# Kernel optimization log

Measured on AMD Instinct MI355X. Metric: run time of the kernel, lower is better.

The kernel has to match this reference:

```python
import jax, jax.numpy as jnp
import numpy as np

N_HEAD = 16

def setup_inputs() -> dict:
    key = jax.random.key(0)
    kx, kq, kk, kv, kp = jax.random.split(key, 5)
    B, T, C = 4, 2048, 1024
    scale = 1.0 / np.sqrt(C)
    x = jax.random.normal(kx, (B, T, C), dtype=jnp.float32)
    Wq = jax.random.normal(kq, (C, C), dtype=jnp.float32) * scale
    Wk = jax.random.normal(kk, (C, C), dtype=jnp.float32) * scale
    Wv = jax.random.normal(kv, (C, C), dtype=jnp.float32) * scale
    Wp = jax.random.normal(kp, (C, C), dtype=jnp.float32) * scale
    return {"x": x, "Wq": Wq, "Wk": Wk, "Wv": Wv, "Wp": Wp}

def reference(x, Wq, Wk, Wv, Wp):
    B, T, C = x.shape
    H = N_HEAD
    D = C // H
    # projections (nn.Linear, no bias): x @ W^T
    q = (x @ Wq.T).reshape(B, T, H, D).transpose(0, 2, 1, 3)  # [B,H,T,D]
    k = (x @ Wk.T).reshape(B, T, H, D).transpose(0, 2, 1, 3)
    v = (x @ Wv.T).reshape(B, T, H, D).transpose(0, 2, 1, 3)
    att = jnp.einsum('bhqd,bhkd->bhqk', q, k) / jnp.sqrt(jnp.float32(D))
    causal = jnp.tril(jnp.ones((T, T), dtype=bool))
    att = jnp.where(causal, att, -jnp.inf)
    att = jax.nn.softmax(att, axis=-1)
    # dropout p=0.0 -> identity
    y = jnp.einsum('bhqk,bhkd->bhqd', att, v)  # [B,H,T,D]
    y = y.transpose(0, 2, 1, 3).reshape(B, T, C)
    return y @ Wp.T
```

## Files before the change

kernel.cpp:

```cpp
#include <hip/hip_runtime.h>

typedef __bf16 bfrag __attribute__((ext_vector_type(8)));
typedef __bf16 bh4 __attribute__((ext_vector_type(4)));
typedef float f4 __attribute__((ext_vector_type(4)));

#define AS1C(p) (const __attribute__((address_space(1))) void*)(p)
#define AS3(p)  (__attribute__((address_space(3))) void*)(p)

#define QSCALE 0.18033688011112042f

__device__ __forceinline__ void g2l16(const __bf16* g, __bf16* l) {
  __builtin_amdgcn_global_load_lds(AS1C(g), AS3(l), 16, 0, 0);
}

__global__ __launch_bounds__(256) void cvt5(
    const float* __restrict__ s0, const float* __restrict__ s1,
    const float* __restrict__ s2, const float* __restrict__ s3,
    const float* __restrict__ s4,
    __bf16* __restrict__ d0, __bf16* __restrict__ d1, __bf16* __restrict__ d2,
    __bf16* __restrict__ d3, __bf16* __restrict__ d4, long n0, long n1) {
  const float* s; __bf16* d; long n;
  switch (blockIdx.y) {
    case 0: s = s0; d = d0; n = n0; break;
    case 1: s = s1; d = d1; n = n1; break;
    case 2: s = s2; d = d2; n = n1; break;
    case 3: s = s3; d = d3; n = n1; break;
    default: s = s4; d = d4; n = n1; break;
  }
  long i = ((long)blockIdx.x * 256 + threadIdx.x) * 8;
  if (i >= n) return;
  float4 a = *(const float4*)(s + i);
  float4 b = *(const float4*)(s + i + 4);
  bfrag o;
  o[0] = (__bf16)a.x; o[1] = (__bf16)a.y; o[2] = (__bf16)a.z; o[3] = (__bf16)a.w;
  o[4] = (__bf16)b.x; o[5] = (__bf16)b.y; o[6] = (__bf16)b.z; o[7] = (__bf16)b.w;
  *(bfrag*)(d + i) = o;
}

#define BARR __builtin_amdgcn_s_barrier()
#define WAIT_LGKM { asm volatile("s_waitcnt lgkmcnt(0)" ::: "memory"); \
                    __builtin_amdgcn_sched_barrier(0); }
#define WAIT_VM(N) asm volatile("s_waitcnt vmcnt(" #N ")" ::: "memory")

template <int MODE>
__global__ __launch_bounds__(512, 2) void gemm_dp(
    const __bf16* __restrict__ A, const __bf16* __restrict__ Bw,
    __bf16* __restrict__ qb, __bf16* __restrict__ kb,
    __bf16* __restrict__ vt, float* __restrict__ Cf, int K) {
  __shared__ __bf16 lds[73728];
  __bf16* ldsA = lds;
  __bf16* ldsB = lds + 24576;
  const int tid = threadIdx.x;
  const int wave = tid >> 6, lane = tid & 63;
  const int lm = lane & 15, quad = lane >> 4;
  const int wm = wave >> 2, wn = wave & 3;
  const int bm = blockIdx.x * 128, bn = blockIdx.y * 256;
  const int srow = lane >> 3;
  const int scol = ((lane & 7) ^ srow) * 8;
  const int rsw = lm & 7;

#define STG_A9(sl, kt) { \
    const __bf16* gp_ = A + (long)(bm + wave * 16 + srow) * K + (kt) * 64 + scol; \
    __bf16* lp_ = ldsA + (sl) * 8192 + wave * 1024 + lane * 8; \
    g2l16(gp_, lp_); g2l16(gp_ + 8 * K, lp_ + 512); }
#define STG_B9(sl, kt, h) { \
    const __bf16* gp_ = Bw + (long)(bn + (h) * 128 + wave * 16 + srow) * K + (kt) * 64 + scol; \
    __bf16* lp_ = ldsB + (sl) * 16384 + (h) * 8192 + wave * 1024 + lane * 8; \
    g2l16(gp_, lp_); g2l16(gp_ + 8 * K, lp_ + 512); }
#define STG_TILE(sl, kt) { STG_A9(sl, kt); STG_B9(sl, kt, 0); STG_B9(sl, kt, 1); }

#define COMPUTE_HALF(sl) { \
    const __bf16* Ab_ = ldsA + (sl) * 8192 + (wm * 64 + lm) * 64; \
    const __bf16* Bb_ = ldsB + (sl) * 16384 + (wn * 64 + lm) * 64; \
    bfrag af_[4][2], bg_[2][2]; \
    _Pragma("unroll") for (int j_ = 0; j_ < 4; ++j_) \
      _Pragma("unroll") for (int kk_ = 0; kk_ < 2; ++kk_) \
        af_[j_][kk_] = *(const bfrag*)(Ab_ + j_ * 1024 + ((kk_ * 4 + quad) ^ rsw) * 8); \
    _Pragma("unroll") for (int n_ = 0; n_ < 2; ++n_) \
      _Pragma("unroll") for (int kk_ = 0; kk_ < 2; ++kk_) \
        bg_[n_][kk_] = *(const bfrag*)(Bb_ + n_ * 1024 + ((kk_ * 4 + quad) ^ rsw) * 8); \
    WAIT_LGKM; \
    __builtin_amdgcn_s_setprio(1); \
    _Pragma("unroll") for (int j_ = 0; j_ < 4; ++j_) \
      _Pragma("unroll") for (int n_ = 0; n_ < 2; ++n_) \
        _Pragma("unroll") for (int kk_ = 0; kk_ < 2; ++kk_) \
          acc[j_][n_] = __builtin_amdgcn_mfma_f32_16x16x32_bf16( \
              af_[j_][kk_], bg_[n_][kk_], acc[j_][n_], 0, 0, 0); \
    __builtin_amdgcn_s_setprio(0); \
    _Pragma("unroll") for (int n_ = 0; n_ < 2; ++n_) \
      _Pragma("unroll") for (int kk_ = 0; kk_ < 2; ++kk_) \
        bg_[n_][kk_] = *(const bfrag*)(Bb_ + (2 + n_) * 1024 + ((kk_ * 4 + quad) ^ rsw) * 8); \
    WAIT_LGKM; \
    __builtin_amdgcn_s_setprio(1); \
    _Pragma("unroll") for (int j_ = 0; j_ < 4; ++j_) \
      _Pragma("unroll") for (int n_ = 0; n_ < 2; ++n_) \
        _Pragma("unroll") for (int kk_ = 0; kk_ < 2; ++kk_) \
          acc[j_][2 + n_] = __builtin_amdgcn_mfma_f32_16x16x32_bf16( \
              af_[j_][kk_], bg_[n_][kk_], acc[j_][2 + n_], 0, 0, 0); \
    __builtin_amdgcn_s_setprio(0); }

  f4 acc[4][4] = {};
  const int ntiles = K >> 6;
  STG_TILE(0, 0);
  STG_TILE(1, 1);
  WAIT_VM(6);
  BARR;
#pragma unroll 1
  for (int i = 0; i < (ntiles >> 1); ++i) {
    const int e = 2 * i, o = 2 * i + 1;
    const int se = e % 3, so = o % 3;
    if (e + 2 < ntiles) { const int s2 = (e + 2) % 3; STG_TILE(s2, e + 2); }
    COMPUTE_HALF(se);
    if (e + 2 < ntiles) { WAIT_VM(6); } else { WAIT_VM(0); }
    BARR;
    if (o + 2 < ntiles) { const int s2 = (o + 2) % 3; STG_TILE(s2, o + 2); }
    COMPUTE_HALF(so);
    if (o + 2 < ntiles) WAIT_VM(6);
    BARR;
  }

  if (MODE == 1) {
#pragma unroll
    for (int mi = 0; mi < 4; ++mi)
#pragma unroll
      for (int ni = 0; ni < 4; ++ni)
#pragma unroll
        for (int r = 0; r < 4; ++r) {
          long row = bm + wm * 64 + mi * 16 + quad * 4 + r;
          long col = bn + wn * 64 + ni * 16 + lm;
          Cf[row * 1024 + col] = acc[mi][ni][r];
        }
  } else if (bn < 2048) {
    __bf16* dst = (bn < 1024) ? qb : kb;
    const float scl = (bn < 1024) ? QSCALE : 1.0f;
    const int nb = bn & 1023;
#pragma unroll
    for (int mi = 0; mi < 4; ++mi)
#pragma unroll
      for (int ni = 0; ni < 4; ++ni)
#pragma unroll
        for (int r = 0; r < 4; ++r) {
          long row = bm + wm * 64 + mi * 16 + quad * 4 + r;
          long col = nb + wn * 64 + ni * 16 + lm;
          dst[row * 1024 + col] = (__bf16)(acc[mi][ni][r] * scl);
        }
  } else {
#pragma unroll
    for (int mi = 0; mi < 4; ++mi)
#pragma unroll
      for (int ni = 0; ni < 4; ++ni)
#pragma unroll
        for (int r = 0; r < 4; ++r) {
          int d = wn * 64 + ni * 16 + lm;
          int tp = wm * 64 + (quad * 4 + r) * 4 + mi;
          lds[d * 130 + tp] = (__bf16)acc[mi][ni][r];
        }
    __syncthreads();
    const int bloc = bm >> 11;
    const int tloc = bm & 2047;
#pragma unroll
    for (int p = 0; p < 8; ++p) {
      int d = (tid >> 4) + p * 32;
      int c = (tid & 15) * 8;
      long dglob = (bn - 2048) + d;
      *(bfrag*)(vt + ((long)bloc * 1024 + dglob) * 2048 + tloc + c) =
          *(const bfrag*)(lds + d * 130 + c);
    }
  }
}

template <bool A_F32, bool OUT_F32>
__global__ __launch_bounds__(256) void gemm_bt_cv(
    const void* __restrict__ Ap, const float* __restrict__ Bp,
    void* __restrict__ Cp, int M, int N, int K, float scl) {
  __shared__ __bf16 As[128 * 32];
  __shared__ __bf16 Bs[128 * 32];
  const int tid = threadIdx.x;
  const int lane = tid & 63, wave = tid >> 6;
  const int lm = lane & 15, quad = lane >> 4;
  const int bm = blockIdx.x * 128, bn = blockIdx.y * 128;
  const int wr = (wave >> 1) * 64, wc = (wave & 1) * 64;
  const int e0 = tid * 16, sr = e0 >> 5, sc = e0 & 31;
  f4 acc[4][4] = {};
  for (int k0 = 0; k0 < K; k0 += 32) {
    if (A_F32) {
      const float4* ga = (const float4*)((const float*)Ap + (long)(bm + sr) * K + k0 + sc);
#pragma unroll
      for (int j = 0; j < 4; ++j) {
        float4 v = ga[j];
        As[sr * 32 + sc + j * 4 + 0] = (__bf16)v.x;
        As[sr * 32 + sc + j * 4 + 1] = (__bf16)v.y;
        As[sr * 32 + sc + j * 4 + 2] = (__bf16)v.z;
        As[sr * 32 + sc + j * 4 + 3] = (__bf16)v.w;
      }
    } else {
      const __bf16* Ab = (const __bf16*)Ap + (long)(bm + sr) * K + k0 + sc;
      *(bfrag*)(As + sr * 32 + sc) = *(const bfrag*)Ab;
      *(bfrag*)(As + sr * 32 + sc + 8) = *(const bfrag*)(Ab + 8);
    }
    {
      const float4* gb = (const float4*)(Bp + (long)(bn + sr) * K + k0 + sc);
#pragma unroll
      for (int j = 0; j < 4; ++j) {
        float4 v = gb[j];
        Bs[sr * 32 + sc + j * 4 + 0] = (__bf16)v.x;
        Bs[sr * 32 + sc + j * 4 + 1] = (__bf16)v.y;
        Bs[sr * 32 + sc + j * 4 + 2] = (__bf16)v.z;
        Bs[sr * 32 + sc + j * 4 + 3] = (__bf16)v.w;
      }
    }
    __syncthreads();
    bfrag af[4], bg[4];
#pragma unroll
    for (int mi = 0; mi < 4; ++mi)
      af[mi] = *(const bfrag*)(As + (wr + mi * 16 + lm) * 32 + quad * 8);
#pragma unroll
    for (int ni = 0; ni < 4; ++ni)
      bg[ni] = *(const bfrag*)(Bs + (wc + ni * 16 + lm) * 32 + quad * 8);
#pragma unroll
    for (int mi = 0; mi < 4; ++mi)
#pragma unroll
      for (int ni = 0; ni < 4; ++ni)
        acc[mi][ni] = __builtin_amdgcn_mfma_f32_16x16x32_bf16(af[mi], bg[ni], acc[mi][ni], 0, 0, 0);
    __syncthreads();
  }
#pragma unroll
  for (int mi = 0; mi < 4; ++mi)
#pragma unroll
    for (int ni = 0; ni < 4; ++ni)
#pragma unroll
      for (int r = 0; r < 4; ++r) {
        long row = bm + wr + mi * 16 + quad * 4 + r;
        long col = bn + wc + ni * 16 + lm;
        if (OUT_F32) ((float*)Cp)[row * N + col] = acc[mi][ni][r] * scl;
        else ((__bf16*)Cp)[row * N + col] = (__bf16)(acc[mi][ni][r] * scl);
      }
}

template <bool VT>
__global__ __launch_bounds__(256, 2) void attn_fwd12(
    const __bf16* Qg, const __bf16* __restrict__ Kg,
    const __bf16* __restrict__ Vsrc, __bf16* Yg) {
  const int TT = 2048, CC = 1024;
  __shared__ __bf16 Ks[64 * 64];
  __shared__ __bf16 Vs[64 * 64];
  __shared__ __bf16 Ps[8 * 1024];
  const int tid = threadIdx.x;
  const int wave = tid >> 6, lane = tid & 63;
  const int lm = lane & 15, quad = lane >> 4;
  const int bh = blockIdx.x;
  const int qt = 15 - blockIdx.y;
  const int b = bh >> 4, h = bh & 15;
  const long rbase = (long)b * TT;
  const int hoff = h * 64;
  int row0[2];
  row0[0] = qt * 128 + wave * 16;
  row0[1] = qt * 128 + 64 + wave * 16;
  __bf16* Pw[2];
#pragma unroll
  for (int fr = 0; fr < 2; ++fr) Pw[fr] = Ps + (wave * 2 + fr) * 1024;
  bfrag qf[2][2];
#pragma unroll
  for (int fr = 0; fr < 2; ++fr)
#pragma unroll
    for (int f = 0; f < 2; ++f)
      qf[fr][f] = *(const bfrag*)(Qg + (rbase + row0[fr] + lm) * CC + hoff + f * 32 + quad * 8);
  bfrag ones;
#pragma unroll
  for (int j = 0; j < 8; ++j) ones[j] = (__bf16)1.0f;
  f4 y[2][4] = {};
  f4 L[2] = {};

  const int psl = ((tid & 7) ^ ((tid >> 3) & 7)) * 8;
  const int rsw = lm & 7;

  const int ktLast = 2 * qt + 1;
  bfrag kin[2], vin[2];
#pragma unroll
  for (int s = 0; s < 2; ++s) {
    int idx = tid + s * 256;
    int r = idx >> 3, c = (idx & 7) * 8;
    kin[s] = *(const bfrag*)(Kg + (rbase + r) * CC + hoff + c);
    if (VT)
      vin[s] = *(const bfrag*)(Vsrc + ((long)b * 1024 + hoff + r) * 2048 + c);
    else
      vin[s] = *(const bfrag*)(Vsrc + (rbase + r) * CC + hoff + c);
  }

  for (int kt = 0; kt <= ktLast; ++kt) {
    const int kBase = kt * 64;
    __syncthreads();
#pragma unroll
    for (int s = 0; s < 2; ++s) {
      int idx = tid + s * 256;
      int r = idx >> 3, c = (idx & 7) * 8;
      *(bfrag*)(Ks + r * 64 + psl) = kin[s];
      if (VT) {
        *(bfrag*)(Vs + r * 64 + psl) = vin[s];
      } else {
        int kp = (r & 15) * 4 + (r >> 4);
#pragma unroll
        for (int j = 0; j < 8; ++j)
          Vs[(c + j) * 64 + ((kp >> 3) ^ ((c + j) & 7)) * 8 + (kp & 7)] = vin[s][j];
      }
    }
    const bool more = (kt < ktLast);
    bfrag kin2[2], vin2[2];
    if (more) {
      const int nB = kBase + 64;
#pragma unroll
      for (int s = 0; s < 2; ++s) {
        int idx = tid + s * 256;
        int r = idx >> 3, c = (idx & 7) * 8;
        kin2[s] = *(const bfrag*)(Kg + (rbase + nB + r) * CC + hoff + c);
        if (VT)
          vin2[s] = *(const bfrag*)(Vsrc + ((long)b * 1024 + hoff + r) * 2048 + nB + c);
        else
          vin2[s] = *(const bfrag*)(Vsrc + (rbase + nB + r) * CC + hoff + c);
      }
    }
    __syncthreads();
    bfrag kf[8];
#pragma unroll
    for (int sub = 0; sub < 4; ++sub)
#pragma unroll
      for (int f = 0; f < 2; ++f)
        kf[sub * 2 + f] = *(const bfrag*)(Ks + (sub * 16 + lm) * 64 + ((f * 4 + quad) ^ rsw) * 8);
#pragma unroll
    for (int fr = 0; fr < 2; ++fr) {
      if (kBase <= row0[fr] + 15) {
        f4 sac[4];
#pragma unroll
        for (int sub = 0; sub < 4; ++sub) {
          f4 z = {};
#pragma unroll
          for (int f = 0; f < 2; ++f)
            z = __builtin_amdgcn_mfma_f32_16x16x32_bf16(qf[fr][f], kf[sub * 2 + f], z, 0, 0, 0);
          sac[sub] = z;
        }
        if (kBase + 63 > row0[fr]) {
#pragma unroll
          for (int r = 0; r < 4; ++r) {
            int prow = quad * 4 + r;
            bh4 pk;
#pragma unroll
            for (int sub = 0; sub < 4; ++sub) {
              float pv = __builtin_amdgcn_exp2f(sac[sub][r]);
              bool masked = (kBase + sub * 16 + lm > row0[fr] + prow);
              pk[sub] = (__bf16)(masked ? 0.f : pv);
            }
            *(bh4*)(Pw[fr] + prow * 64 + ((lm >> 1) ^ (prow & 7)) * 8 + (lm & 1) * 4) = pk;
          }
        } else {
#pragma unroll
          for (int r = 0; r < 4; ++r) {
            int prow = quad * 4 + r;
            bh4 pk;
#pragma unroll
            for (int sub = 0; sub < 4; ++sub)
              pk[sub] = (__bf16)__builtin_amdgcn_exp2f(sac[sub][r]);
            *(bh4*)(Pw[fr] + prow * 64 + ((lm >> 1) ^ (prow & 7)) * 8 + (lm & 1) * 4) = pk;
          }
        }
      }
    }
    __asm__ volatile("s_waitcnt lgkmcnt(0)" ::: "memory");
    bfrag vf[8];
#pragma unroll
    for (int sub = 0; sub < 4; ++sub)
#pragma unroll
      for (int f = 0; f < 2; ++f)
        vf[sub * 2 + f] = *(const bfrag*)(Vs + (sub * 16 + lm) * 64 + ((f * 4 + quad) ^ rsw) * 8);
#pragma unroll
    for (int fr = 0; fr < 2; ++fr) {
      if (kBase <= row0[fr] + 15) {
#pragma unroll
        for (int f = 0; f < 2; ++f) {
          bfrag pf = *(const bfrag*)(Pw[fr] + lm * 64 + ((f * 4 + quad) ^ rsw) * 8);
          L[fr] = __builtin_amdgcn_mfma_f32_16x16x32_bf16(pf, ones, L[fr], 0, 0, 0);
#pragma unroll
          for (int ds = 0; ds < 4; ++ds)
            y[fr][ds] = __builtin_amdgcn_mfma_f32_16x16x32_bf16(pf, vf[ds * 2 + f], y[fr][ds], 0, 0, 0);
        }
      }
    }
    if (more) {
      kin[0] = kin2[0]; kin[1] = kin2[1];
      vin[0] = vin2[0]; vin[1] = vin2[1];
    }
  }
#pragma unroll
  for (int fr = 0; fr < 2; ++fr)
#pragma unroll
    for (int ds = 0; ds < 4; ++ds)
#pragma unroll
      for (int r = 0; r < 4; ++r) {
        long row = rbase + row0[fr] + quad * 4 + r;
        Yg[row * CC + hoff + ds * 16 + lm] = (__bf16)(y[fr][ds][r] / L[fr][r]);
      }
}

extern "C" void kernel_launch(void* const* d_in, const int* in_sizes, int n_in,
                              void* d_out, int out_size, void* d_ws, size_t ws_size,
                              hipStream_t stream) {
  (void)in_sizes; (void)n_in; (void)out_size;
  const float* x  = (const float*)d_in[0];
  const float* Wq = (const float*)d_in[1];
  const float* Wk = (const float*)d_in[2];
  const float* Wv = (const float*)d_in[3];
  const float* Wp = (const float*)d_in[4];
  float* out = (float*)d_out;
  const long R = 8192;
  const long BUF = R * 1024;
  const long WN = 1024L * 1024;
  __bf16* qb = (__bf16*)d_ws;
  __bf16* kb = (__bf16*)d_out;
  __bf16* vslot = kb + BUF;
  dim3 blk(256, 1, 1);
  const size_t need = (size_t)(2 * BUF + 4 * WN) * 2;
  if (ws_size >= need) {
    __bf16* xb = qb + BUF;
    __bf16* wqkv = xb + BUF;
    __bf16* wpb = wqkv + 3 * WN;
    cvt5<<<dim3((unsigned)(BUF / (256 * 8)), 5, 1), blk, 0, stream>>>(
        x, Wq, Wk, Wv, Wp, xb, wqkv, wqkv + WN, wqkv + 2 * WN, wpb, BUF, WN);
    gemm_dp<0><<<dim3(64, 12, 1), dim3(512, 1, 1), 0, stream>>>(
        xb, wqkv, qb, kb, vslot, nullptr, 1024);
    attn_fwd12<true><<<dim3(64, 16, 1), blk, 0, stream>>>(qb, kb, vslot, qb);
    gemm_dp<1><<<dim3(64, 4, 1), dim3(512, 1, 1), 0, stream>>>(
        qb, wpb, nullptr, nullptr, nullptr, out, 1024);
  } else {
    gemm_bt_cv<true, false><<<dim3(64, 8, 1), blk, 0, stream>>>(x, Wq, qb, 8192, 1024, 1024, QSCALE);
    gemm_bt_cv<true, false><<<dim3(64, 8, 1), blk, 0, stream>>>(x, Wk, kb, 8192, 1024, 1024, 1.0f);
    gemm_bt_cv<true, false><<<dim3(64, 8, 1), blk, 0, stream>>>(x, Wv, vslot, 8192, 1024, 1024, 1.0f);
    attn_fwd12<false><<<dim3(64, 16, 1), blk, 0, stream>>>(qb, kb, vslot, qb);
    gemm_bt_cv<false, true><<<dim3(64, 8, 1), blk, 0, stream>>>(qb, Wp, out, 8192, 1024, 1024, 1.0f);
  }
}
```

Measured before the change: 233.3 us.

## Pair mirrored causal query tiles per 512-thread attention block for load balance

The attention kernel now uses 512 threads (8 waves) per block, and each block handles two query tiles, i and 15-i, so every block does roughly equal causal work. The grid halves to 8 tiles in y. K/V staging now takes one 16-byte load per thread instead of two, and the P scratch buffer doubles. The goal is to remove tail imbalance from the triangular workload and to share each K/V tile load across both query tiles. The cost is more LDS per block and possibly lower occupancy.

```diff
diff --git a/kernel.cpp b/kernel.cpp
--- a/kernel.cpp
+++ b/kernel.cpp
@@ -238,24 +238,24 @@
 }
 
 template <bool VT>
-__global__ __launch_bounds__(256, 2) void attn_fwd12(
+__global__ __launch_bounds__(512, 2) void attn_fwd13(
     const __bf16* Qg, const __bf16* __restrict__ Kg,
     const __bf16* __restrict__ Vsrc, __bf16* Yg) {
   const int TT = 2048, CC = 1024;
   __shared__ __bf16 Ks[64 * 64];
   __shared__ __bf16 Vs[64 * 64];
-  __shared__ __bf16 Ps[8 * 1024];
+  __shared__ __bf16 Ps[16 * 1024];
   const int tid = threadIdx.x;
   const int wave = tid >> 6, lane = tid & 63;
   const int lm = lane & 15, quad = lane >> 4;
-  const int bh = blockIdx.x;
-  const int qt = 15 - blockIdx.y;
+  const int bh = blockIdx.x, i = blockIdx.y;
   const int b = bh >> 4, h = bh & 15;
+  const int qtA = i, qtB = 15 - i;
   const long rbase = (long)b * TT;
   const int hoff = h * 64;
   int row0[2];
-  row0[0] = qt * 128 + wave * 16;
-  row0[1] = qt * 128 + 64 + wave * 16;
+  row0[0] = qtA * 128 + wave * 16;
+  row0[1] = qtB * 128 + wave * 16;
   __bf16* Pw[2];
 #pragma unroll
   for (int fr = 0; fr < 2; ++fr) Pw[fr] = Ps + (wave * 2 + fr) * 1024;
@@ -274,50 +274,36 @@
   const int psl = ((tid & 7) ^ ((tid >> 3) & 7)) * 8;
   const int rsw = lm & 7;
 
-  const int ktLast = 2 * qt + 1;
-  bfrag kin[2], vin[2];
-#pragma unroll
-  for (int s = 0; s < 2; ++s) {
-    int idx = tid + s * 256;
-    int r = idx >> 3, c = (idx & 7) * 8;
-    kin[s] = *(const bfrag*)(Kg + (rbase + r) * CC + hoff + c);
-    if (VT)
-      vin[s] = *(const bfrag*)(Vsrc + ((long)b * 1024 + hoff + r) * 2048 + c);
-    else
-      vin[s] = *(const bfrag*)(Vsrc + (rbase + r) * CC + hoff + c);
-  }
+  const int ktLast = 2 * qtB + 1;
+  const int sr = tid >> 3, scc = (tid & 7) * 8;
+  bfrag kin, vin;
+  kin = *(const bfrag*)(Kg + (rbase + sr) * CC + hoff + scc);
+  if (VT)
+    vin = *(const bfrag*)(Vsrc + ((long)b * 1024 + hoff + sr) * 2048 + scc);
+  else
+    vin = *(const bfrag*)(Vsrc + (rbase + sr) * CC + hoff + scc);
 
   for (int kt = 0; kt <= ktLast; ++kt) {
     const int kBase = kt * 64;
     __syncthreads();
-#pragma unroll
-    for (int s = 0; s < 2; ++s) {
-      int idx = tid + s * 256;
-      int r = idx >> 3, c = (idx & 7) * 8;
-      *(bfrag*)(Ks + r * 64 + psl) = kin[s];
-      if (VT) {
-        *(bfrag*)(Vs + r * 64 + psl) = vin[s];
-      } else {
-        int kp = (r & 15) * 4 + (r >> 4);
-#pragma unroll
-        for (int j = 0; j < 8; ++j)
-          Vs[(c + j) * 64 + ((kp >> 3) ^ ((c + j) & 7)) * 8 + (kp & 7)] = vin[s][j];
-      }
+    *(bfrag*)(Ks + sr * 64 + psl) = kin;
+    if (VT) {
+      *(bfrag*)(Vs + sr * 64 + psl) = vin;
+    } else {
+      int kp = (sr & 15) * 4 + (sr >> 4);
+#pragma unroll
+      for (int j = 0; j < 8; ++j)
+        Vs[(scc + j) * 64 + ((kp >> 3) ^ ((scc + j) & 7)) * 8 + (kp & 7)] = vin[j];
     }
     const bool more = (kt < ktLast);
-    bfrag kin2[2], vin2[2];
+    bfrag kin2, vin2;
     if (more) {
       const int nB = kBase + 64;
-#pragma unroll
-      for (int s = 0; s < 2; ++s) {
-        int idx = tid + s * 256;
-        int r = idx >> 3, c = (idx & 7) * 8;
-        kin2[s] = *(const bfrag*)(Kg + (rbase + nB + r) * CC + hoff + c);
-        if (VT)
-          vin2[s] = *(const bfrag*)(Vsrc + ((long)b * 1024 + hoff + r) * 2048 + nB + c);
-        else
-          vin2[s] = *(const bfrag*)(Vsrc + (rbase + nB + r) * CC + hoff + c);
-      }
+      kin2 = *(const bfrag*)(Kg + (rbase + nB + sr) * CC + hoff + scc);
+      if (VT)
+        vin2 = *(const bfrag*)(Vsrc + ((long)b * 1024 + hoff + sr) * 2048 + nB + scc);
+      else
+        vin2 = *(const bfrag*)(Vsrc + (rbase + nB + sr) * CC + hoff + scc);
     }
     __syncthreads();
     bfrag kf[8];
@@ -384,10 +370,7 @@
         }
       }
     }
-    if (more) {
-      kin[0] = kin2[0]; kin[1] = kin2[1];
-      vin[0] = vin2[0]; vin[1] = vin2[1];
-    }
+    if (more) { kin = kin2; vin = vin2; }
   }
 #pragma unroll
   for (int fr = 0; fr < 2; ++fr)
@@ -426,14 +409,14 @@
         x, Wq, Wk, Wv, Wp, xb, wqkv, wqkv + WN, wqkv + 2 * WN, wpb, BUF, WN);
     gemm_dp<0><<<dim3(64, 12, 1), dim3(512, 1, 1), 0, stream>>>(
         xb, wqkv, qb, kb, vslot, nullptr, 1024);
-    attn_fwd12<true><<<dim3(64, 16, 1), blk, 0, stream>>>(qb, kb, vslot, qb);
+    attn_fwd13<true><<<dim3(64, 8, 1), dim3(512, 1, 1), 0, stream>>>(qb, kb, vslot, qb);
     gemm_dp<1><<<dim3(64, 4, 1), dim3(512, 1, 1), 0, stream>>>(
         qb, wpb, nullptr, nullptr, nullptr, out, 1024);
   } else {
     gemm_bt_cv<true, false><<<dim3(64, 8, 1), blk, 0, stream>>>(x, Wq, qb, 8192, 1024, 1024, QSCALE);
     gemm_bt_cv<true, false><<<dim3(64, 8, 1), blk, 0, stream>>>(x, Wk, kb, 8192, 1024, 1024, 1.0f);
     gemm_bt_cv<true, false><<<dim3(64, 8, 1), blk, 0, stream>>>(x, Wv, vslot, 8192, 1024, 1024, 1.0f);
-    attn_fwd12<false><<<dim3(64, 16, 1), blk, 0, stream>>>(qb, kb, vslot, qb);
+    attn_fwd13<false><<<dim3(64, 8, 1), dim3(512, 1, 1), 0, stream>>>(qb, kb, vslot, qb);
     gemm_bt_cv<false, true><<<dim3(64, 8, 1), blk, 0, stream>>>(qb, Wp, out, 8192, 1024, 1024, 1.0f);
   }
 }
```

Result: faster. 227.2 us (-2.6%).
